# Kernel optimization log

Hardware: AMD Instinct MI355X
Metric: run time of the kernel (lower is better)

## Reference

```python
import jax, jax.numpy as jnp
import numpy as np

B, T, D = 4, 2048, 1024
C_BIAS = 0.0  # init kwarg c
LN_EPS = 1e-5


def setup_inputs() -> dict:
    key = jax.random.key(0)
    ks = jax.random.split(key, 8)
    s = 1.0 / np.sqrt(D)
    return {
        "x": jax.random.normal(ks[0], (B, T, D), dtype=jnp.float32),
        "l": jax.random.randint(ks[1], (B,), 1, T + 1),  # lengths in [1, T]
        "Wq": jax.random.normal(ks[2], (D, D), dtype=jnp.float32) * s,
        "Wk": jax.random.normal(ks[3], (D, D), dtype=jnp.float32) * s,
        "Wv": jax.random.normal(ks[4], (D, D), dtype=jnp.float32) * s,
        "Wo": jax.random.normal(ks[5], (D, D), dtype=jnp.float32) * s,
        "bo": jnp.zeros((D,), dtype=jnp.float32),
        "gamma": jnp.ones((D,), dtype=jnp.float32),
        "beta": jnp.zeros((D,), dtype=jnp.float32),
    }


def reference(x, l, Wq, Wk, Wv, Wo, bo, gamma, beta):
    # LayerNorm over last dim
    mu = jnp.mean(x, axis=-1, keepdims=True)
    var = jnp.mean(jnp.square(x - mu), axis=-1, keepdims=True)
    x_norm = (x - mu) * jax.lax.rsqrt(var + LN_EPS) * gamma + beta

    # QKV projections (torch Linear: y = x @ W.T, no bias)
    q = jnp.einsum("btd,ed->bte", x_norm, Wq)
    k = jnp.einsum("btd,ed->bte", x_norm, Wk)
    v = jnp.einsum("btd,ed->bte", x_norm, Wv)

    scale = 1.0 / jnp.sqrt(jnp.float32(D))
    scores = C_BIAS + jnp.einsum("bid,bjd->bij", q, k) * scale  # [B,T,T]

    # Mask is applied along the ROW (dim 1) axis, and softmax is over dim 1
    # (faithful to the original: mask.unsqueeze(2) + Softmax(dim=1)).
    valid_rows = jnp.arange(T)[None, :] < l[:, None]  # [B,T]
    scores = jnp.where(valid_rows[:, :, None], scores, -jnp.inf)
    attn = jax.nn.softmax(scores, axis=1)  # normalize over rows

    y = x + jnp.einsum("bij,bjd->bid", attn, v)
    out = jax.nn.relu(jnp.einsum("btd,ed->bte", y, Wo) + bo)
    return out
```

## Files before the change

### kernel.cpp

```cpp
#include <hip/hip_runtime.h>
#include <hip/hip_fp16.h>

typedef unsigned short u16;
typedef __attribute__((ext_vector_type(8))) short bf16x8;
typedef __attribute__((ext_vector_type(4))) float f32x4;

#define T_SEQ 2048
#define DIM 1024
#define NB 4
#define NCH 16
#define RCHUNK (T_SEQ / NCH)

__device__ __forceinline__ u16 f2bf(float f) {
  union { float f; unsigned u; } c; c.f = f;
  unsigned r = c.u + 0x7fffu + ((c.u >> 16) & 1u);
  return (u16)(r >> 16);
}

__device__ __forceinline__ void gload_lds16(const void* g, void* l) {
  __builtin_amdgcn_global_load_lds((const __attribute__((address_space(1))) void*)g,
                                   (__attribute__((address_space(3))) void*)l, 16, 0, 0);
}

#define SBAR() asm volatile("s_barrier" ::: "memory")
#define VMCNT0() asm volatile("s_waitcnt vmcnt(0)" ::: "memory")
#define VMCNT3() asm volatile("s_waitcnt vmcnt(3)" ::: "memory")
#define VMCNT4() asm volatile("s_waitcnt vmcnt(4)" ::: "memory")

__global__ __launch_bounds__(256) void ln_kernel(const float* __restrict__ x,
                                                 const float* __restrict__ gamma,
                                                 const float* __restrict__ beta,
                                                 u16* __restrict__ xn) {
  const int row = blockIdx.x;
  const int tid = threadIdx.x;
  const float4 v = *(const float4*)(x + (size_t)row * DIM + tid * 4);
  float s  = v.x + v.y + v.z + v.w;
  float ss = v.x * v.x + v.y * v.y + v.z * v.z + v.w * v.w;
#pragma unroll
  for (int o = 32; o > 0; o >>= 1) { s += __shfl_down(s, o); ss += __shfl_down(ss, o); }
  __shared__ float rs[4], rss[4];
  const int wid = tid >> 6, lane = tid & 63;
  if (lane == 0) { rs[wid] = s; rss[wid] = ss; }
  __syncthreads();
  s  = rs[0] + rs[1] + rs[2] + rs[3];
  ss = rss[0] + rss[1] + rss[2] + rss[3];
  const float mu = s * (1.f / DIM);
  const float var = ss * (1.f / DIM) - mu * mu;
  const float rstd = rsqrtf(var + 1e-5f);
  const float4 g  = *(const float4*)(gamma + tid * 4);
  const float4 be = *(const float4*)(beta + tid * 4);
  ushort4 o;
  o.x = f2bf((v.x - mu) * rstd * g.x + be.x);
  o.y = f2bf((v.y - mu) * rstd * g.y + be.y);
  o.z = f2bf((v.z - mu) * rstd * g.z + be.z);
  o.w = f2bf((v.w - mu) * rstd * g.w + be.w);
  *(ushort4*)(xn + (size_t)row * DIM + tid * 4) = o;
}

__global__ __launch_bounds__(256) void wcvt4(const float* __restrict__ wq,
                                             const float* __restrict__ wk,
                                             const float* __restrict__ wv,
                                             const float* __restrict__ wo,
                                             u16* __restrict__ dqk,
                                             u16* __restrict__ dv,
                                             u16* __restrict__ dw) {
  const int sel = blockIdx.x >> 10;
  const size_t t = (size_t)(blockIdx.x & 1023) * 256 + threadIdx.x;
  const float* w = (sel == 0) ? wq : (sel == 1) ? wk : (sel == 2) ? wv : wo;
  u16* d = (sel == 0) ? dqk : (sel == 1) ? (dqk + 1048576) : (sel == 2) ? dv : dw;
  const float4 v = *(const float4*)(w + t * 4);
  ushort4 u; u.x = f2bf(v.x); u.y = f2bf(v.y); u.z = f2bf(v.z); u.w = f2bf(v.w);
  *(ushort4*)(d + t * 4) = u;
}

template <int EPI, int BM>
__global__ __launch_bounds__(512, 2) void gemm_bt(
    const u16* __restrict__ A, const u16* __restrict__ B, void* __restrict__ Cv,
    int K, int lda, int ldb, int ldc,
    long sA, long sB, long sC,
    const float* __restrict__ aux, long sAux, float scale) {
  constexpr int MI = BM / 32;
  __shared__ __align__(16) u16 As[4][BM * 32];
  __shared__ __align__(16) u16 Bs[4][256 * 32];
  const int bz = blockIdx.z;
  const u16* Ab = A + (size_t)bz * sA;
  const u16* Bb = B + (size_t)bz * sB;

  const int nb = gridDim.x * gridDim.y;
  int bid = blockIdx.y * gridDim.x + blockIdx.x;
  bid = (bid & 7) * (nb >> 3) + (bid >> 3);
  const int gx = gridDim.x;
  const int tileN = (bid % gx) * 256;
  const int tileM = (bid / gx) * BM;

  const int t = threadIdx.x;
  const int lane = t & 63;
  const int wid = t >> 6;
  const int wm = wid >> 2, wn = wid & 3;

  const int srow = t >> 2;
  const int qsw = (((t & 3) ^ (srow & 3) ^ ((srow >> 2) & 3))) * 8;
  const size_t aoff0 = (size_t)(tileM + srow) * lda + qsw;
  const size_t aoff1 = (size_t)(tileM + 128 + srow) * lda + qsw;
  const size_t boff0 = (size_t)(tileN + srow) * ldb + qsw;
  const size_t boff1 = (size_t)(tileN + 128 + srow) * ldb + qsw;

  const int frow = lane & 15;
  const int kg = lane >> 4;
  const int ckk = ((kg ^ (lane & 3) ^ ((lane >> 2) & 3))) * 8;

  f32x4 acc[MI][4] = {};
  const int NT = K >> 5;

#pragma unroll
  for (int p = 0; p < 2; ++p) {
    const size_t kp = (size_t)p << 5;
    gload_lds16(Ab + aoff0 + kp, &As[p][t * 8]);
    gload_lds16(Bb + boff0 + kp, &Bs[p][t * 8]);
    if constexpr (BM == 256) gload_lds16(Ab + aoff1 + kp, &As[p][4096 + t * 8]);
    gload_lds16(Bb + boff1 + kp, &Bs[p][4096 + t * 8]);
  }
  if constexpr (BM == 256) VMCNT4(); else VMCNT3();
  SBAR();

  for (int tau = 0; tau < NT; ++tau) {
    const int cur = tau & 3;
    const int nxt = (tau + 2) & 3;
    const bool st = (tau + 2 < NT);
    const size_t k0 = (size_t)(tau + 2) << 5;

    bf16x8 af[4], bf[4];
#pragma unroll
    for (int j = 0; j < 4; ++j)
      bf[j] = *(const bf16x8*)&Bs[cur][(wn * 64 + j * 16 + frow) * 32 + ckk];
#pragma unroll
    for (int i = 0; i < 4; ++i)
      af[i] = *(const bf16x8*)&As[cur][(wm * (BM / 2) + i * 16 + frow) * 32 + ckk];
    if (st) {
      gload_lds16(Ab + aoff0 + k0, &As[nxt][t * 8]);
      gload_lds16(Bb + boff0 + k0, &Bs[nxt][t * 8]);
      if constexpr (BM == 128) gload_lds16(Bb + boff1 + k0, &Bs[nxt][4096 + t * 8]);
    }
    if constexpr (BM == 128) { if (st) VMCNT3(); else VMCNT0(); }
    SBAR();
    __builtin_amdgcn_s_setprio(1);
#pragma unroll
    for (int i = 0; i < 4; ++i)
#pragma unroll
      for (int j = 0; j < 4; ++j)
        acc[i][j] = __builtin_amdgcn_mfma_f32_16x16x32_bf16(af[i], bf[j], acc[i][j], 0, 0, 0);
    __builtin_amdgcn_s_setprio(0);

    if constexpr (BM == 256) {
      bf16x8 af2[4];
#pragma unroll
      for (int i = 0; i < 4; ++i)
        af2[i] = *(const bf16x8*)&As[cur][(wm * 128 + (4 + i) * 16 + frow) * 32 + ckk];
      if (st) {
        gload_lds16(Ab + aoff1 + k0, &As[nxt][4096 + t * 8]);
        gload_lds16(Bb + boff1 + k0, &Bs[nxt][4096 + t * 8]);
      }
      if (st) VMCNT4(); else VMCNT0();
      SBAR();
      __builtin_amdgcn_s_setprio(1);
#pragma unroll
      for (int i = 0; i < 4; ++i)
#pragma unroll
        for (int j = 0; j < 4; ++j)
          acc[4 + i][j] = __builtin_amdgcn_mfma_f32_16x16x32_bf16(af2[i], bf[j], acc[4 + i][j], 0, 0, 0);
      __builtin_amdgcn_s_setprio(0);
    }
  }

  const int r0 = tileM + wm * (BM / 2) + (kg << 2);
  const int c0 = tileN + wn * 64 + frow;
#pragma unroll
  for (int i = 0; i < MI; ++i)
#pragma unroll
    for (int j = 0; j < 4; ++j)
#pragma unroll
      for (int r = 0; r < 4; ++r) {
        const int row = r0 + i * 16 + r, col = c0 + j * 16;
        const size_t idx = (size_t)row * ldc + col;
        float v = acc[i][j][r];
        if constexpr (EPI == 0) {
          ((u16*)Cv + (size_t)bz * sC)[idx] = f2bf(v);
        } else if constexpr (EPI == 1) {
          ((__half*)Cv + (size_t)bz * sC)[idx] = __float2half(v * scale);
        } else if constexpr (EPI == 2) {
          v += (aux + (size_t)bz * sAux)[idx];
          ((u16*)Cv + (size_t)bz * sC)[idx] = f2bf(v);
        } else {
          v += aux[col];
          ((float*)Cv + (size_t)bz * sC)[idx] = fmaxf(v, 0.f);
        }
      }
}

__global__ __launch_bounds__(256) void colreduce_part(const __half* __restrict__ S,
                                                      const int* __restrict__ l,
                                                      float* __restrict__ mp,
                                                      float* __restrict__ zp) {
  const int b = blockIdx.y;
  const int ch = blockIdx.z;
  const int j = blockIdx.x * 256 + threadIdx.x;
  const __half* Sb = S + (size_t)b * T_SEQ * T_SEQ;
  const int L = l[b];
  const int i0 = ch * RCHUNK;
  const int i1 = min(i0 + RCHUNK, L);

  float mm[4] = {-1e30f, -1e30f, -1e30f, -1e30f};
  float zz[4] = {0.f, 0.f, 0.f, 0.f};
  for (int i = i0; i < i1; i += 4) {
#pragma unroll
    for (int u = 0; u < 4; ++u) {
      const int ii = i + u;
      if (ii < i1) {
        const float s = __half2float(Sb[(size_t)ii * T_SEQ + j]);
        if (s > mm[u]) { zz[u] *= __expf(mm[u] - s); mm[u] = s; zz[u] += 1.f; }
        else           { zz[u] += __expf(s - mm[u]); }
      }
    }
  }
  float M = fmaxf(fmaxf(mm[0], mm[1]), fmaxf(mm[2], mm[3]));
  float Z = 0.f;
#pragma unroll
  for (int u = 0; u < 4; ++u) Z += zz[u] * __expf(mm[u] - M);

  const size_t o = ((size_t)ch * NB + b) * T_SEQ + j;
  mp[o] = M;
  zp[o] = Z;
}

__global__ __launch_bounds__(256) void colreduce_comb(const float* __restrict__ mp,
                                                      const float* __restrict__ zp,
                                                      float* __restrict__ m,
                                                      float* __restrict__ rz) {
  const int b = blockIdx.y;
  const int j = blockIdx.x * 256 + threadIdx.x;
  float M = -1e30f, Z = 0.f;
#pragma unroll
  for (int c = 0; c < NCH; ++c) {
    const size_t o = ((size_t)c * NB + b) * T_SEQ + j;
    const float mc = mp[o], zc = zp[o];
    const float nm = fmaxf(M, mc);
    Z = Z * __expf(M - nm) + zc * __expf(mc - nm);
    M = nm;
  }
  m[b * T_SEQ + j] = M;
  rz[b * T_SEQ + j] = 1.f / Z;
}

__global__ __launch_bounds__(256) void pbuild(const __half* __restrict__ S,
                                              const int* __restrict__ l,
                                              const float* __restrict__ m,
                                              const float* __restrict__ rz,
                                              u16* __restrict__ P) {
  const int b = blockIdx.x >> 11;
  const int i = blockIdx.x & (T_SEQ - 1);
  const int j0 = threadIdx.x * 8;
  const size_t off = ((size_t)blockIdx.x << 11) + j0;
  ushort4 o0, o1;
  if (i < l[b]) {
    const __half* sp = S + off;
    const float* mp = m + b * T_SEQ + j0;
    const float* zp = rz + b * T_SEQ + j0;
    u16 tmp[8];
#pragma unroll
    for (int t = 0; t < 8; ++t)
      tmp[t] = f2bf(__expf(__half2float(sp[t]) - mp[t]) * zp[t]);
    o0 = make_ushort4(tmp[0], tmp[1], tmp[2], tmp[3]);
    o1 = make_ushort4(tmp[4], tmp[5], tmp[6], tmp[7]);
  } else {
    o0 = make_ushort4(0, 0, 0, 0);
    o1 = make_ushort4(0, 0, 0, 0);
  }
  *(ushort4*)(P + off) = o0;
  *(ushort4*)(P + off + 4) = o1;
}

extern "C" void kernel_launch(void* const* d_in, const int* in_sizes, int n_in,
                              void* d_out, int out_size, void* d_ws, size_t ws_size,
                              hipStream_t stream) {
  (void)in_sizes; (void)n_in; (void)out_size; (void)ws_size;
  const float* x     = (const float*)d_in[0];
  const int*   l     = (const int*)d_in[1];
  const float* Wq    = (const float*)d_in[2];
  const float* Wk    = (const float*)d_in[3];
  const float* Wv    = (const float*)d_in[4];
  const float* Wo    = (const float*)d_in[5];
  const float* bo    = (const float*)d_in[6];
  const float* gamma = (const float*)d_in[7];
  const float* beta  = (const float*)d_in[8];

  char* ws = (char*)d_ws;
  const size_t MiB = 1024 * 1024;
  u16* xn   = (u16*)(ws);
  u16* wqkb = (u16*)(ws + 16 * MiB);
  u16* wvb  = (u16*)(ws + 20 * MiB);
  u16* wob  = (u16*)(ws + 22 * MiB);
  u16* QKb  = (u16*)(ws + 24 * MiB);
  u16* Vt   = (u16*)(ws + 56 * MiB);
  float* mpart = (float*)(ws + 20 * MiB);
  float* zpart = (float*)(ws + 20 * MiB + 512 * 1024);
  float* mb  = (float*)(ws + 72 * MiB);
  float* rzb = (float*)(ws + 72 * MiB + 32 * 1024);
  u16* Pb = QKb;
  u16* yb = xn;
  __half* S = (__half*)d_out;
  float* outp = (float*)d_out;

  const long TD = (long)T_SEQ * DIM, TT = (long)T_SEQ * T_SEQ;
  const long TQK = (long)T_SEQ * 2048;

  ln_kernel<<<NB * T_SEQ, 256, 0, stream>>>(x, gamma, beta, xn);
  wcvt4<<<4096, 256, 0, stream>>>(Wq, Wk, Wv, Wo, wqkb, wvb, wob);

  gemm_bt<0, 256><<<dim3(8, 32, 1), 512, 0, stream>>>(
      xn, wqkb, QKb, DIM, DIM, DIM, 2048, 0, 0, 0, nullptr, 0, 0.f);
  gemm_bt<0, 128><<<dim3(32, 8, 1), 512, 0, stream>>>(
      wvb, xn, Vt, DIM, DIM, DIM, 8192, 0, 0, 0, nullptr, 0, 0.f);
  gemm_bt<1, 256><<<dim3(8, 8, NB), 512, 0, stream>>>(
      QKb, QKb + 1024, S, DIM, 2048, 2048, T_SEQ, TQK, TQK, TT, nullptr, 0, 0.03125f);
  colreduce_part<<<dim3(T_SEQ / 256, NB, NCH), 256, 0, stream>>>(S, l, mpart, zpart);
  colreduce_comb<<<dim3(T_SEQ / 256, NB), 256, 0, stream>>>(mpart, zpart, mb, rzb);
  pbuild<<<NB * T_SEQ, 256, 0, stream>>>(S, l, mb, rzb, Pb);
  gemm_bt<2, 128><<<dim3(4, 16, NB), 512, 0, stream>>>(
      Pb, Vt, yb, T_SEQ, T_SEQ, 8192, DIM, TT, 2048, TD, x, TD, 0.f);
  gemm_bt<3, 128><<<dim3(4, 64, 1), 512, 0, stream>>>(
      yb, wob, outp, DIM, DIM, DIM, DIM, 0, 0, 0, bo, 0, 0.f);
}
```

Before: 246.2 us.

## Fuse column softmax partial stats into score GEMM and deepen prefetch pipeline

```diff
diff --git a/kernel.cpp b/kernel.cpp
--- a/kernel.cpp
+++ b/kernel.cpp
@@ -8,8 +8,7 @@
 #define T_SEQ 2048
 #define DIM 1024
 #define NB 4
-#define NCH 16
-#define RCHUNK (T_SEQ / NCH)
+#define NCH 8
 
 __device__ __forceinline__ u16 f2bf(float f) {
   union { float f; unsigned u; } c; c.f = f;
@@ -23,9 +22,7 @@
 }
 
 #define SBAR() asm volatile("s_barrier" ::: "memory")
-#define VMCNT0() asm volatile("s_waitcnt vmcnt(0)" ::: "memory")
-#define VMCNT3() asm volatile("s_waitcnt vmcnt(3)" ::: "memory")
-#define VMCNT4() asm volatile("s_waitcnt vmcnt(4)" ::: "memory")
+#define WVL(n) asm volatile("s_waitcnt vmcnt(" n ") lgkmcnt(0)" ::: "memory")
 
 __global__ __launch_bounds__(256) void ln_kernel(const float* __restrict__ x,
                                                  const float* __restrict__ gamma,
@@ -78,7 +75,8 @@
     const u16* __restrict__ A, const u16* __restrict__ B, void* __restrict__ Cv,
     int K, int lda, int ldb, int ldc,
     long sA, long sB, long sC,
-    const float* __restrict__ aux, long sAux, float scale) {
+    const float* __restrict__ aux, long sAux, float scale,
+    const int* __restrict__ lptr, float* __restrict__ mpQ, float* __restrict__ zpQ) {
   constexpr int MI = BM / 32;
   __shared__ __align__(16) u16 As[4][BM * 32];
   __shared__ __align__(16) u16 Bs[4][256 * 32];
@@ -113,21 +111,22 @@
   const int NT = K >> 5;
 
 #pragma unroll
-  for (int p = 0; p < 2; ++p) {
+  for (int p = 0; p < 3; ++p) {
     const size_t kp = (size_t)p << 5;
     gload_lds16(Ab + aoff0 + kp, &As[p][t * 8]);
     gload_lds16(Bb + boff0 + kp, &Bs[p][t * 8]);
     if constexpr (BM == 256) gload_lds16(Ab + aoff1 + kp, &As[p][4096 + t * 8]);
     gload_lds16(Bb + boff1 + kp, &Bs[p][4096 + t * 8]);
   }
-  if constexpr (BM == 256) VMCNT4(); else VMCNT3();
+  if constexpr (BM == 256) { asm volatile("s_waitcnt vmcnt(8)" ::: "memory"); }
+  else                     { asm volatile("s_waitcnt vmcnt(6)" ::: "memory"); }
   SBAR();
 
   for (int tau = 0; tau < NT; ++tau) {
     const int cur = tau & 3;
-    const int nxt = (tau + 2) & 3;
-    const bool st = (tau + 2 < NT);
-    const size_t k0 = (size_t)(tau + 2) << 5;
+    const int tgt = (tau + 3) & 3;
+    const bool st = (tau + 3 < NT);
+    const size_t k0 = (size_t)(tau + 3) << 5;
 
     bf16x8 af[4], bf[4];
 #pragma unroll
@@ -137,11 +136,13 @@
     for (int i = 0; i < 4; ++i)
       af[i] = *(const bf16x8*)&As[cur][(wm * (BM / 2) + i * 16 + frow) * 32 + ckk];
     if (st) {
-      gload_lds16(Ab + aoff0 + k0, &As[nxt][t * 8]);
-      gload_lds16(Bb + boff0 + k0, &Bs[nxt][t * 8]);
-      if constexpr (BM == 128) gload_lds16(Bb + boff1 + k0, &Bs[nxt][4096 + t * 8]);
-    }
-    if constexpr (BM == 128) { if (st) VMCNT3(); else VMCNT0(); }
+      gload_lds16(Ab + aoff0 + k0, &As[tgt][t * 8]);
+      gload_lds16(Bb + boff0 + k0, &Bs[tgt][t * 8]);
+      if constexpr (BM == 128) gload_lds16(Bb + boff1 + k0, &Bs[tgt][4096 + t * 8]);
+    }
+    if constexpr (BM == 128) {
+      if (tau < NT - 3) WVL("6"); else if (tau == NT - 3) WVL("3"); else WVL("0");
+    }
     SBAR();
     __builtin_amdgcn_s_setprio(1);
 #pragma unroll
@@ -157,10 +158,10 @@
       for (int i = 0; i < 4; ++i)
         af2[i] = *(const bf16x8*)&As[cur][(wm * 128 + (4 + i) * 16 + frow) * 32 + ckk];
       if (st) {
-        gload_lds16(Ab + aoff1 + k0, &As[nxt][4096 + t * 8]);
-        gload_lds16(Bb + boff1 + k0, &Bs[nxt][4096 + t * 8]);
+        gload_lds16(Ab + aoff1 + k0, &As[tgt][4096 + t * 8]);
+        gload_lds16(Bb + boff1 + k0, &Bs[tgt][4096 + t * 8]);
       }
-      if (st) VMCNT4(); else VMCNT0();
+      if (tau < NT - 3) WVL("8"); else if (tau == NT - 3) WVL("4"); else WVL("0");
       SBAR();
       __builtin_amdgcn_s_setprio(1);
 #pragma unroll
@@ -195,41 +196,53 @@
           ((float*)Cv + (size_t)bz * sC)[idx] = fmaxf(v, 0.f);
         }
       }
-}
-
-__global__ __launch_bounds__(256) void colreduce_part(const __half* __restrict__ S,
-                                                      const int* __restrict__ l,
-                                                      float* __restrict__ mp,
-                                                      float* __restrict__ zp) {
-  const int b = blockIdx.y;
-  const int ch = blockIdx.z;
-  const int j = blockIdx.x * 256 + threadIdx.x;
-  const __half* Sb = S + (size_t)b * T_SEQ * T_SEQ;
-  const int L = l[b];
-  const int i0 = ch * RCHUNK;
-  const int i1 = min(i0 + RCHUNK, L);
-
-  float mm[4] = {-1e30f, -1e30f, -1e30f, -1e30f};
-  float zz[4] = {0.f, 0.f, 0.f, 0.f};
-  for (int i = i0; i < i1; i += 4) {
-#pragma unroll
-    for (int u = 0; u < 4; ++u) {
-      const int ii = i + u;
-      if (ii < i1) {
-        const float s = __half2float(Sb[(size_t)ii * T_SEQ + j]);
-        if (s > mm[u]) { zz[u] *= __expf(mm[u] - s); mm[u] = s; zz[u] += 1.f; }
-        else           { zz[u] += __expf(s - mm[u]); }
+
+  if constexpr (EPI == 1) {
+    const int L = lptr[bz];
+    __shared__ float2 red[2][4][4][16];
+    float Ms[4], Zs[4];
+#pragma unroll
+    for (int j = 0; j < 4; ++j) {
+      float mj = -3e38f;
+#pragma unroll
+      for (int i = 0; i < MI; ++i)
+#pragma unroll
+        for (int r = 0; r < 4; ++r) {
+          const int row = r0 + i * 16 + r;
+          if (row < L) mj = fmaxf(mj, acc[i][j][r] * scale);
+        }
+      mj = fmaxf(mj, __shfl_xor(mj, 16, 64));
+      mj = fmaxf(mj, __shfl_xor(mj, 32, 64));
+      float zj = 0.f;
+#pragma unroll
+      for (int i = 0; i < MI; ++i)
+#pragma unroll
+        for (int r = 0; r < 4; ++r) {
+          const int row = r0 + i * 16 + r;
+          if (row < L) zj += __expf(acc[i][j][r] * scale - mj);
+        }
+      zj += __shfl_xor(zj, 16, 64);
+      zj += __shfl_xor(zj, 32, 64);
+      Ms[j] = mj; Zs[j] = zj;
+    }
+    if (lane < 16) {
+#pragma unroll
+      for (int j = 0; j < 4; ++j) red[wm][wn][j][frow] = make_float2(Ms[j], Zs[j]);
+    }
+    __syncthreads();
+    if (wm == 0 && lane < 16) {
+#pragma unroll
+      for (int j = 0; j < 4; ++j) {
+        const float2 a = red[0][wn][j][frow];
+        const float2 b = red[1][wn][j][frow];
+        const float M = fmaxf(a.x, b.x);
+        const float Z = a.y * __expf(a.x - M) + b.y * __expf(b.x - M);
+        const int col = tileN + wn * 64 + j * 16 + frow;
+        const size_t o = ((size_t)(tileM >> 8) * NB + bz) * T_SEQ + col;
+        mpQ[o] = M; zpQ[o] = Z;
       }
     }
   }
-  float M = fmaxf(fmaxf(mm[0], mm[1]), fmaxf(mm[2], mm[3]));
-  float Z = 0.f;
-#pragma unroll
-  for (int u = 0; u < 4; ++u) Z += zz[u] * __expf(mm[u] - M);
-
-  const size_t o = ((size_t)ch * NB + b) * T_SEQ + j;
-  mp[o] = M;
-  zp[o] = Z;
 }
 
 __global__ __launch_bounds__(256) void colreduce_comb(const float* __restrict__ mp,
@@ -238,7 +251,7 @@
                                                       float* __restrict__ rz) {
   const int b = blockIdx.y;
   const int j = blockIdx.x * 256 + threadIdx.x;
-  float M = -1e30f, Z = 0.f;
+  float M = -3e38f, Z = 0.f;
 #pragma unroll
   for (int c = 0; c < NCH; ++c) {
     const size_t o = ((size_t)c * NB + b) * T_SEQ + j;
@@ -317,16 +330,20 @@
   wcvt4<<<4096, 256, 0, stream>>>(Wq, Wk, Wv, Wo, wqkb, wvb, wob);
 
   gemm_bt<0, 256><<<dim3(8, 32, 1), 512, 0, stream>>>(
-      xn, wqkb, QKb, DIM, DIM, DIM, 2048, 0, 0, 0, nullptr, 0, 0.f);
+      xn, wqkb, QKb, DIM, DIM, DIM, 2048, 0, 0, 0, nullptr, 0, 0.f,
+      nullptr, nullptr, nullptr);
   gemm_bt<0, 128><<<dim3(32, 8, 1), 512, 0, stream>>>(
-      wvb, xn, Vt, DIM, DIM, DIM, 8192, 0, 0, 0, nullptr, 0, 0.f);
+      wvb, xn, Vt, DIM, DIM, DIM, 8192, 0, 0, 0, nullptr, 0, 0.f,
+      nullptr, nullptr, nullptr);
   gemm_bt<1, 256><<<dim3(8, 8, NB), 512, 0, stream>>>(
-      QKb, QKb + 1024, S, DIM, 2048, 2048, T_SEQ, TQK, TQK, TT, nullptr, 0, 0.03125f);
-  colreduce_part<<<dim3(T_SEQ / 256, NB, NCH), 256, 0, stream>>>(S, l, mpart, zpart);
+      QKb, QKb + 1024, S, DIM, 2048, 2048, T_SEQ, TQK, TQK, TT, nullptr, 0, 0.03125f,
+      l, mpart, zpart);
   colreduce_comb<<<dim3(T_SEQ / 256, NB), 256, 0, stream>>>(mpart, zpart, mb, rzb);
   pbuild<<<NB * T_SEQ, 256, 0, stream>>>(S, l, mb, rzb, Pb);
   gemm_bt<2, 128><<<dim3(4, 16, NB), 512, 0, stream>>>(
-      Pb, Vt, yb, T_SEQ, T_SEQ, 8192, DIM, TT, 2048, TD, x, TD, 0.f);
+      Pb, Vt, yb, T_SEQ, T_SEQ, 8192, DIM, TT, 2048, TD, x, TD, 0.f,
+      nullptr, nullptr, nullptr);
   gemm_bt<3, 128><<<dim3(4, 64, 1), 512, 0, stream>>>(
-      yb, wob, outp, DIM, DIM, DIM, DIM, 0, 0, 0, bo, 0, 0.f);
-}
+      yb, wob, outp, DIM, DIM, DIM, DIM, 0, 0, 0, bo, 0, 0.f,
+      nullptr, nullptr, nullptr);
+}
```

Measured after the change: 210.0 us. 14.7% less time.
